# Kernel tuning notes

Hardware: AMD Instinct MI355X
Metric: run time of the kernel (lower is better)

## Reference

```python
import jax, jax.numpy as jnp
import numpy as np

# ---------------- Chu-Liu-Edmonds MST decode (faithful numpy port) ----------------

def _find_cycle(parents, length, current_nodes):
    added = [False] * length
    added[0] = True
    cycle = set()
    has_cycle = False
    for i in range(1, length):
        if has_cycle:
            break
        if added[i] or not current_nodes[i]:
            continue
        this_cycle = {i}
        added[i] = True
        has_cycle = True
        next_node = i
        while parents[next_node] not in this_cycle:
            next_node = parents[next_node]
            if added[next_node]:
                has_cycle = False
                break
            added[next_node] = True
            this_cycle.add(next_node)
        if has_cycle:
            original = next_node
            cycle.add(original)
            next_node = parents[original]
            while next_node != original:
                cycle.add(next_node)
                next_node = parents[next_node]
            break
    return has_cycle, list(cycle)


def chu_liu_edmonds(length, score_matrix, current_nodes, final_edges, old_input, old_output, representatives):
    parents = [-1]
    for node1 in range(1, length):
        parents.append(0)
        if current_nodes[node1]:
            max_score = score_matrix[0, node1]
            for node2 in range(1, length):
                if node2 == node1 or not current_nodes[node2]:
                    continue
                new_score = score_matrix[node2, node1]
                if new_score > max_score:
                    max_score = new_score
                    parents[node1] = node2
    has_cycle, cycle = _find_cycle(parents, length, current_nodes)
    if not has_cycle:
        final_edges[0] = -1
        for node in range(1, length):
            if not current_nodes[node]:
                continue
            parent = old_input[parents[node], node]
            child = old_output[parents[node], node]
            final_edges[child] = parent
        return
    cycle_weight = 0.0
    for node in cycle:
        cycle_weight += score_matrix[parents[node], node]
    cycle_representative = cycle[0]
    for node in range(length):
        if not current_nodes[node] or node in cycle:
            continue
        in_edge_weight = float('-inf')
        in_edge = -1
        out_edge_weight = float('-inf')
        out_edge = -1
        for node_in_cycle in cycle:
            if score_matrix[node_in_cycle, node] > in_edge_weight:
                in_edge_weight = score_matrix[node_in_cycle, node]
                in_edge = node_in_cycle
            score = cycle_weight + score_matrix[node, node_in_cycle] - score_matrix[parents[node_in_cycle], node_in_cycle]
            if score > out_edge_weight:
                out_edge_weight = score
                out_edge = node_in_cycle
        score_matrix[cycle_representative, node] = in_edge_weight
        old_input[cycle_representative, node] = old_input[in_edge, node]
        old_output[cycle_representative, node] = old_output[in_edge, node]
        score_matrix[node, cycle_representative] = out_edge_weight
        old_output[node, cycle_representative] = old_output[node, out_edge]
        old_input[node, cycle_representative] = old_input[node, out_edge]
    considered = []
    for i, node_in_cycle in enumerate(cycle):
        considered.append(set())
        if i > 0:
            current_nodes[node_in_cycle] = False
        for node in representatives[node_in_cycle]:
            considered[i].add(node)
            if i > 0:
                representatives[cycle_representative].add(node)
    chu_liu_edmonds(length, score_matrix, current_nodes, final_edges, old_input, old_output, representatives)
    found = False
    key_node = -1
    for i, node in enumerate(cycle):
        for cycle_rep in considered[i]:
            if cycle_rep in final_edges:
                key_node = node
                found = True
                break
        if found:
            break
    previous = parents[key_node]
    while previous != key_node:
        child = old_output[parents[previous], previous]
        parent = old_input[parents[previous], previous]
        final_edges[child] = parent
        previous = parents[previous]


def decode_mst(energy, length):
    # energy: numpy [num_labels, T, T]
    max_length = energy.shape[-1]
    energy = energy[:, :length, :length]
    label_id_matrix = energy.argmax(axis=0)
    score_matrix = np.array(energy.max(axis=0), copy=True)
    old_input = np.zeros([length, length], dtype=np.int32)
    old_output = np.zeros([length, length], dtype=np.int32)
    current_nodes = [True] * length
    representatives = []
    for node1 in range(length):
        score_matrix[node1, node1] = 0.0
        representatives.append({node1})
        for node2 in range(node1 + 1, length):
            old_input[node1, node2] = node1
            old_output[node1, node2] = node2
            old_input[node2, node1] = node2
            old_output[node2, node1] = node1
    final_edges = {}
    chu_liu_edmonds(length, score_matrix, current_nodes, final_edges, old_input, old_output, representatives)
    heads = np.zeros([max_length], np.int32)
    head_type = np.ones([max_length], np.int32)
    for child, parent in final_edges.items():
        heads[child] = parent
        head_type[child] = label_id_matrix[parent, child]
    return heads, head_type


# ---------------- biaffine scoring (jax) ----------------

@jax.jit
def _energy(encoded_text, W_head_arc, b_head_arc, W_dep_arc, b_dep_arc, U_arc,
            W_head_lab, b_head_lab, W_dep_lab, b_dep_lab, U_lab):
    h_arc = jax.nn.elu(encoded_text @ W_head_arc + b_head_arc)   # [B,T,A]
    d_arc = jax.nn.elu(encoded_text @ W_dep_arc + b_dep_arc)     # [B,T,A]
    arc_scores = jnp.einsum('bia,ac,bjc->bij', h_arc, U_arc, d_arc)  # head i -> dep j
    h_lab = jax.nn.elu(encoded_text @ W_head_lab + b_head_lab)   # [B,T,R]
    d_lab = jax.nn.elu(encoded_text @ W_dep_lab + b_dep_lab)     # [B,T,R]
    lab_scores = jnp.einsum('bir,lrs,bjs->blij', h_lab, U_lab, d_lab)  # [B,L,T,T]
    norm_arc = jax.nn.log_softmax(arc_scores, axis=1)   # normalize over heads
    norm_lab = jax.nn.log_softmax(lab_scores, axis=1)   # normalize over labels
    return jnp.exp(norm_arc[:, None, :, :] + norm_lab)  # [B,L,T,T] edge energies


def setup_inputs() -> dict:
    key = jax.random.key(0)
    ks = jax.random.split(key, 8)
    B, T, D, A, R, L = 32, 128, 768, 512, 128, 50
    s = 0.02
    return {
        'encoded_text': jax.random.normal(ks[0], (B, T, D), jnp.float32),
        'W_head_arc': jax.random.normal(ks[1], (D, A), jnp.float32) * s,
        'b_head_arc': jnp.zeros((A,), jnp.float32),
        'W_dep_arc': jax.random.normal(ks[2], (D, A), jnp.float32) * s,
        'b_dep_arc': jnp.zeros((A,), jnp.float32),
        'U_arc': jax.random.normal(ks[3], (A, A), jnp.float32) * s,
        'W_head_lab': jax.random.normal(ks[4], (D, R), jnp.float32) * s,
        'b_head_lab': jnp.zeros((R,), jnp.float32),
        'W_dep_lab': jax.random.normal(ks[5], (D, R), jnp.float32) * s,
        'b_dep_lab': jnp.zeros((R,), jnp.float32),
        'U_lab': jax.random.normal(ks[6], (L, R, R), jnp.float32) * s,
        'mask': jnp.ones((B, T), jnp.bool_),
    }


def reference(encoded_text, W_head_arc, b_head_arc, W_dep_arc, b_dep_arc, U_arc,
              W_head_lab, b_head_lab, W_dep_lab, b_dep_lab, U_lab, mask):
    energy = _energy(encoded_text, W_head_arc, b_head_arc, W_dep_arc, b_dep_arc, U_arc,
                     W_head_lab, b_head_lab, W_dep_lab, b_dep_lab, U_lab)
    lengths = np.asarray(mask.sum(-1))
    energy_np = np.asarray(energy)
    heads, tags = [], []
    # per-example Chu-Liu-Edmonds decode (inherently sequential, as in the original)
    for i in range(energy_np.shape[0]):
        h, t = decode_mst(energy_np[i], int(lengths[i]))
        heads.append(h)
        tags.append(t)
    return energy, jnp.asarray(np.stack(heads)), jnp.asarray(np.stack(tags))
```

## Files before the change

### kernel.cpp

```cpp
#include <hip/hip_runtime.h>
#include <math.h>

#define B_ 32
#define T_ 128
#define D_ 768
#define A_ 512
#define R_ 128
#define L_ 50

__global__ __launch_bounds__(256)
void proj_gemm_k(const float* __restrict__ X,
                 const float* __restrict__ Wha, const float* __restrict__ bha,
                 const float* __restrict__ Wda, const float* __restrict__ bda,
                 const float* __restrict__ Whl, const float* __restrict__ bhl,
                 const float* __restrict__ Wdl, const float* __restrict__ bdl,
                 float* __restrict__ HA, float* __restrict__ DA,
                 float* __restrict__ HL, float* __restrict__ DL)
{
    __shared__ float As[16][68];
    __shared__ float Bs[16][132];
    const int bx = blockIdx.x;
    const float *W, *bias; float* C; int ld, ncol;
    if (bx < 4)      { W = Wha; bias = bha; C = HA; ld = 512; ncol = bx * 128; }
    else if (bx < 8) { W = Wda; bias = bda; C = DA; ld = 512; ncol = (bx - 4) * 128; }
// ... 165 lines not shown
    for (int i = 0; i < T_; ++i) base[(size_t)i * T_] -= ls;
}

__global__ __launch_bounds__(256)
void lab_inplace_k(float* __restrict__ E, const float* __restrict__ dlt)
{
    __shared__ __align__(16) float As[T_ * R_];
    int l = blockIdx.x, b = blockIdx.y;
    float* base = E + ((size_t)b * L_ + l) * T_ * T_;
    int tid = threadIdx.x;
#pragma unroll
    for (int it = 0; it < 16; ++it) {
        int idx = (it * 256 + tid) * 4;
        *(float4*)&As[idx] = *(const float4*)&base[idx];
    }
    __syncthreads();
    int tx = tid & 15, ty = tid >> 4;
    int j0 = tx * 8, i0 = ty * 8;
    const float* dl = dlt + (size_t)b * T_ * R_;
    float acc[8][8] = {};
    for (int s0 = 0; s0 < R_; s0 += 4) {
        float a[8][4], bb[4][8];
#pragma unroll
        for (int ii = 0; ii < 8; ++ii) {
            float4 v = *(const float4*)&As[(i0 + ii) * R_ + s0];
            a[ii][0] = v.x; a[ii][1] = v.y; a[ii][2] = v.z; a[ii][3] = v.w;
        }
#pragma unroll
        for (int ss = 0; ss < 4; ++ss) {
            float4 x = *(const float4*)&dl[(size_t)(s0 + ss) * T_ + j0];
            float4 y = *(const float4*)&dl[(size_t)(s0 + ss) * T_ + j0 + 4];
            bb[ss][0] = x.x; bb[ss][1] = x.y; bb[ss][2] = x.z; bb[ss][3] = x.w;
            bb[ss][4] = y.x; bb[ss][5] = y.y; bb[ss][6] = y.z; bb[ss][7] = y.w;
        }
#pragma unroll
        for (int ii = 0; ii < 8; ++ii)
#pragma unroll
            for (int jj = 0; jj < 8; ++jj)
#pragma unroll
                for (int ss = 0; ss < 4; ++ss)
                    acc[ii][jj] += a[ii][ss] * bb[ss][jj];
    }
#pragma unroll
    for (int ii = 0; ii < 8; ++ii) {
        float4 o0 = { acc[ii][0], acc[ii][1], acc[ii][2], acc[ii][3] };
        float4 o1 = { acc[ii][4], acc[ii][5], acc[ii][6], acc[ii][7] };
        *(float4*)&base[(size_t)(i0 + ii) * T_ + j0] = o0;
        *(float4*)&base[(size_t)(i0 + ii) * T_ + j0 + 4] = o1;
    }
}

__global__ __launch_bounds__(256)
void energy_combine_k(float* __restrict__ E, const float* __restrict__ narc,
                      float* __restrict__ score_g, unsigned char* __restrict__ labmax_g)
{
    int g = blockIdx.x * 256 + threadIdx.x;
    int b = g >> 14;
    int ij = g & 16383;
    float* base = E + (size_t)b * L_ * T_ * T_ + ij;
    float v[L_];
    float m = -INFINITY;
    int am = 0;
#pragma unroll
    for (int l = 0; l < L_; ++l) {
        v[l] = base[(size_t)l * T_ * T_];
        if (v[l] > m) { m = v[l]; am = l; }
    }
    float s = 0.0f;
#pragma unroll
    for (int l = 0; l < L_; ++l) s += expf(v[l] - m);
    float ls = m + logf(s);
    float na = narc[(size_t)b * T_ * T_ + ij];
#pragma unroll
    for (int l = 0; l < L_; ++l) base[(size_t)l * T_ * T_] = expf(na + v[l] - ls);
    int i = ij >> 7, j = ij & 127;
    score_g[(size_t)b * 16384 + ij] = (i == j) ? 0.0f : expf(na + m - ls);
    labmax_g[(size_t)b * 16384 + ij] = (unsigned char)am;
}

__global__ __launch_bounds__(256)
void mst_k(const float* __restrict__ score_g, const unsigned char* __restrict__ labmax_g,
           float* __restrict__ heads, float* __restrict__ tags)
{
    int b = blockIdx.x, t = threadIdx.x;
    __shared__ float score[128 * 128];
    __shared__ unsigned char oin[128 * 128];
    __shared__ unsigned char oout[128 * 128];
    __shared__ unsigned char pstL[128 * 128];
    __shared__ unsigned char tstL[128 * 128];
    __shared__ unsigned char cstL[128 * 128];
    __shared__ int parents[128];
    __shared__ int fe[128];
    __shared__ float pmx[128];
    __shared__ int pp[128];
    __shared__ float sub[128];
    __shared__ unsigned char cyc[128], oncyc[128], pstrow[128];

    volatile float* vscore = score;
    volatile int* vpar = parents;
    volatile int* vfe = fe;
    volatile unsigned char* vcyc = cyc;
    volatile unsigned char* voncyc = oncyc;
    volatile unsigned char* voin = oin;
    volatile unsigned char* voout = oout;
    volatile unsigned char* vpstrow = pstrow;
    volatile float* vsub = sub;
    volatile unsigned char* vcst = cstL;
    volatile unsigned char* vpst = pstL;
    volatile unsigned char* vtst = tstL;

    {
        const float4* src = (const float4*)(score_g + (size_t)b * 16384);
#pragma unroll
        for (int r = 0; r < 16; ++r)
            ((float4*)score)[r * 256 + t] = src[r * 256 + t];
    }
    {
        int row = t >> 1, half = t & 1;
        unsigned int tv = (unsigned int)row * 0x01010101u;
        unsigned int* oinw = (unsigned int*)&oin[row * 128];
        unsigned int* ooutw = (unsigned int*)&oout[row * 128];
#pragma unroll
        for (int w = 0; w < 16; ++w) {
            int idx = half * 16 + w;
            oinw[idx] = tv;
            ooutw[idx] = 0x03020100u + 0x04040404u * (unsigned int)idx;
        }
    }
    if (t < 128) { fe[t] = -2; oncyc[t] = 0; }
    __syncthreads();
    if (t < 128) {
        score[t * 128 + t] = -INFINITY;
        oin[t * 129] = 0; oout[t * 129] = 0;
    }
    __syncthreads();
    float mxl = 0.0f; int pl = 0;
    if (t >= 128) {
        int col = t - 128;
        float mx = -INFINITY; int pu = 64;
        if (col != 0) {
            mx = score[64 * 128 + col];
#pragma unroll 16
            for (int n2 = 65; n2 < 128; ++n2) {
                float sc = score[n2 * 128 + col];
                if (sc > mx) { mx = sc; pu = n2; }
            }
        }
        pmx[col] = mx; pp[col] = pu;
    } else if (t != 0) {
        mxl = score[t]; pl = 0;
#pragma unroll 16
        for (int n2 = 1; n2 < 64; ++n2) {
            float sc = score[n2 * 128 + t];
            if (sc > mxl) { mxl = sc; pl = n2; }
        }
    }
    __syncthreads();
    if (t == 0) parents[0] = -1;
    else if (t < 128) parents[t] = (pmx[t] > mxl) ? pp[t] : pl;
    __syncthreads();

    if (t < 64) {
        const int n0 = t, n1 = t + 64;
        int p0 = vpar[n0], p1 = vpar[n1];
        int c0 = 1, c1 = 1;
        int r0 = n0, r1 = n1;
        int lev = 0;
        int nact = 128;
        for (;;) {
            int rounds = 32 - __clz(nact - 1);
            int a0 = (n0 == 0 || !c0) ? 0 : p0;
            int a1 = (!c1) ? 0 : p1;
            int m0 = n0, m1 = n1;
            for (int s = 0; s < rounds; ++s) {
                int pk0 = (a0 << 7) | m0;
                int pk1 = (a1 << 7) | m1;
                int s0l = a0 & 63, s1l = a1 & 63;
                int q00 = __shfl(pk0, s0l, 64);
                int q01 = __shfl(pk1, s0l, 64);
                int q10 = __shfl(pk0, s1l, 64);
                int q11 = __shfl(pk1, s1l, 64);
                int g0 = (a0 & 64) ? q01 : q00;
                int g1 = (a1 & 64) ? q11 : q10;
                a0 = g0 >> 7; int gm0 = g0 & 127; m0 = gm0 < m0 ? gm0 : m0;
                a1 = g1 >> 7; int gm1 = g1 & 127; m1 = gm1 < m1 ? gm1 : m1;
            }
            int pred0 = (n0 >= 1) && c0 && (a0 != 0);
            int pred1 = c1 && (a1 != 0);
            unsigned long long bal0 = __ballot(pred0);
            unsigned long long bal1 = __ballot(pred1);
            if (bal0 == 0ull && bal1 == 0ull) {
                if (n0 == 0) vfe[0] = -1;
                else if (c0) {
                    int pa = voin[p0 * 128 + n0];
                    int ch = voout[p0 * 128 + n0];
                    vfe[ch] = pa;
                }
                if (c1) {
                    int pa = voin[p1 * 128 + n1];
                    int ch = voout[p1 * 128 + n1];
                    vfe[ch] = pa;
                }
                __threadfence_block();
                break;
            }
            unsigned char ep = (unsigned char)(lev + 1);
            if (pred0) voncyc[a0] = ep;
            if (pred1) voncyc[a1] = ep;
            __threadfence_block();
            int onc0 = (voncyc[n0] == ep);
            int onc1 = (voncyc[n1] == ep);
            unsigned long long ob0 = __ballot(onc0);
            unsigned long long ob1 = __ballot(onc1);
            const int rep = ob0 ? ((int)__ffsll((long long)ob0) - 1)
                                : (64 + (int)__ffsll((long long)ob1) - 1);
            int member0 = onc0 && (m0 == rep);
            int member1 = onc1 && (m1 == rep);
            unsigned long long mb0 = __ballot(member0);
            unsigned long long mb1 = __ballot(member1);
            int clen = (int)__popcll(mb0) + (int)__popcll(mb1);
            int rank0 = (int)__popcll(mb0 & ((1ull << n0) - 1ull));
            int rank1 = (int)__popcll(mb0) + (int)__popcll(mb1 & ((1ull << n0) - 1ull));
            float s0m = member0 ? vscore[p0 * 128 + n0] : 0.0f;
            float s1m = member1 ? vscore[p1 * 128 + n1] : 0.0f;
            if (member0) { vcyc[rank0] = (unsigned char)n0; vsub[rank0] = s0m;
                           vcst[lev * 128 + rank0] = (unsigned char)n0; }
            if (member1) { vcyc[rank1] = (unsigned char)n1; vsub[rank1] = s1m;
                           vcst[lev * 128 + rank1] = (unsigned char)n1; }
            vpst[lev * 128 + n0] = (unsigned char)p0;
            vpst[lev * 128 + n1] = (unsigned char)p1;
            int mbit_r0 = (r0 < 64) ? (int)((mb0 >> r0) & 1ull) : (int)((mb1 >> (r0 - 64)) & 1ull);
            int mbit_r1 = (r1 < 64) ? (int)((mb0 >> r1) & 1ull) : (int)((mb1 >> (r1 - 64)) & 1ull);
            int tg0 = mbit_r0 ? ((r0 < 64) ? (int)__popcll(mb0 & ((1ull << r0) - 1ull))
                                           : (int)__popcll(mb0) + (int)__popcll(mb1 & ((1ull << (r0 - 64)) - 1ull)))
                              : 0xFF;
            int tg1 = mbit_r1 ? ((r1 < 64) ? (int)__popcll(mb0 & ((1ull << r1) - 1ull))
                                           : (int)__popcll(mb0) + (int)__popcll(mb1 & ((1ull << (r1 - 64)) - 1ull)))
                              : 0xFF;
            vtst[lev * 128 + n0] = (unsigned char)tg0;
            vtst[lev * 128 + n1] = (unsigned char)tg1;
            __threadfence_block();
            float cw = 0.0f;
            for (int i = 0; i < clen; ++i) cw += vsub[i];
#pragma unroll
            for (int half = 0; half < 2; ++half) {
                int n = half ? n1 : n0;
                int cc = half ? c1 : c0;
                int mem = half ? member1 : member0;
                if (cc && !mem) {
                    float inw = -INFINITY, outw = -INFINITY;
                    int ine = 0, oute = 0;
                    for (int i = 0; i < clen; ++i) {
                        int nic = (int)vcyc[i];
                        float sb = vsub[i];
                        float si = vscore[nic * 128 + n];
                        if (si > inw) { inw = si; ine = nic; }
                        float so = cw + vscore[n * 128 + nic] - sb;
                        if (so > outw) { outw = so; oute = nic; }
                    }
                    vscore[rep * 128 + n] = inw;
                    voin[rep * 128 + n] = voin[ine * 128 + n];
                    voout[rep * 128 + n] = voout[ine * 128 + n];
                    vscore[n * 128 + rep] = outw;
                    voout[n * 128 + rep] = voout[n * 128 + oute];
                    voin[n * 128 + rep] = voin[n * 128 + oute];
                }
            }
            __threadfence_block();
            if (member0 && n0 != rep) c0 = 0;
            if (member1 && n1 != rep) c1 = 0;
            if (tg0 != 0xFF) r0 = rep;
            if (tg1 != 0xFF) r1 = rep;
            int mbit_p0 = (p0 < 64) ? (int)((mb0 >> p0) & 1ull) : (int)((mb1 >> (p0 - 64)) & 1ull);
            int mbit_p1 = (p1 < 64) ? (int)((mb0 >> p1) & 1ull) : (int)((mb1 >> (p1 - 64)) & 1ull);
            if (c0 && n0 != 0 && n0 != rep && mbit_p0) p0 = rep;
            if (c1 && n1 != rep && mbit_p1) p1 = rep;
            {
                float cv0 = c0 ? vscore[n0 * 128 + rep] : -INFINITY;
                float cv1 = c1 ? vscore[n1 * 128 + rep] : -INFINITY;
                float bv; int bi;
                if (cv1 > cv0) { bv = cv1; bi = n1; } else { bv = cv0; bi = n0; }
#pragma unroll
                for (int off = 32; off >= 1; off >>= 1) {
                    float ov = __shfl_xor(bv, off, 64);
                    int oi = __shfl_xor(bi, off, 64);
                    if (ov > bv || (ov == bv && oi < bi)) { bv = ov; bi = oi; }
                }
                if (n0 == rep) p0 = bi;
                if (n1 == rep) p1 = bi;
            }
            nact -= (clen - 1);
            ++lev;
        }
        for (int l2 = lev - 1; l2 >= 0; --l2) {
            int q0 = vpst[l2 * 128 + n0], q1 = vpst[l2 * 128 + n1];
            vpstrow[n0] = (unsigned char)q0;
            vpstrow[n1] = (unsigned char)q1;
            int tg0 = vtst[l2 * 128 + n0], tg1 = vtst[l2 * 128 + n1];
            int kf0 = (tg0 != 0xFF) && (vfe[n0] != -2);
            int kf1 = (tg1 != 0xFF) && (vfe[n1] != -2);
            int kv0 = kf0 ? (int)vcst[l2 * 128 + tg0] : 0;
            int kv1 = kf1 ? (int)vcst[l2 * 128 + tg1] : 0;
            unsigned long long kb0 = __ballot(kf0);
            unsigned long long kb1 = __ballot(kf1);
            int key = -1;
            if (kb0)      key = __shfl(kv0, (int)__ffsll((long long)kb0) - 1, 64);
            else if (kb1) key = __shfl(kv1, (int)__ffsll((long long)kb1) - 1, 64);
            __threadfence_block();
            if (t == 0 && key >= 0) {
                int prev = (int)vpstrow[key];
                int guard = 0;
                while (prev != key && guard++ < 200) {
                    int pp2 = (int)vpstrow[prev];
                    int ch = (int)voout[pp2 * 128 + prev];
                    int pa = (int)voin[pp2 * 128 + prev];
                    vfe[ch] = pa;
                    prev = pp2;
                }
            }
            __threadfence_block();
        }
    }
    __syncthreads();

    if (t < 128) {
        int f = fe[t];
        float h, ht;
        if (f != -2) {
            h = (float)f;
            int prow = (f < 0) ? 127 : f;
            ht = (float)(int)labmax_g[(size_t)b * 16384 + prow * 128 + t];
        } else { h = 0.0f; ht = 1.0f; }
        heads[b * 128 + t] = h;
        tags[b * 128 + t] = ht;
    }
}

extern "C" void kernel_launch(void* const* d_in, const int* in_sizes, int n_in,
                              void* d_out, int out_size, void* d_ws, size_t ws_size,
                              hipStream_t stream)
{
    const float* X   = (const float*)d_in[0];
    const float* Wha = (const float*)d_in[1];
    const float* bha = (const float*)d_in[2];
    const float* Wda = (const float*)d_in[3];
    const float* bda = (const float*)d_in[4];
    const float* Ua  = (const float*)d_in[5];
    const float* Whl = (const float*)d_in[6];
    const float* bhl = (const float*)d_in[7];
    const float* Wdl = (const float*)d_in[8];
    const float* bdl = (const float*)d_in[9];
    const float* Ul  = (const float*)d_in[10];

    char* ws = (char*)d_ws;
    float* HA    = (float*)(ws + (size_t)0);
    float* DA    = (float*)(ws + ((size_t)8 << 20));
    float* TA    = (float*)(ws + ((size_t)16 << 20));
    float* HL    = (float*)(ws + ((size_t)24 << 20));
    float* DL    = (float*)(ws + ((size_t)26 << 20));
    float* DLt   = (float*)(ws + ((size_t)28 << 20));
    float* ARC   = (float*)(ws + ((size_t)30 << 20));
    float* SCORE = (float*)(ws + ((size_t)32 << 20));
    unsigned char* LABMAX = (unsigned char*)(ws + ((size_t)34 << 20));

    float* E     = (float*)d_out;
    float* heads = E + (size_t)B_ * L_ * T_ * T_;
    float* tags  = heads + (size_t)B_ * T_;

    dim3 thr(256);
    proj_gemm_k<<<dim3(10, 64), thr, 0, stream>>>(X, Wha, bha, Wda, bda, Whl, bhl, Wdl, bdl,
                                                  HA, DA, HL, DL);
    gemm_k<<<dim3(4, 64, 1), thr, 0, stream>>>(HA, Ua, nullptr, TA, 512, 512, 512, 512, 0, 0, 0, (long long)128 * 512, 0);
    transpose_k<<<dim3(4, 4, 32), dim3(32, 8), 0, stream>>>(DL, DLt);
    gemm_k<<<dim3(1, 2, 32), thr, 0, stream>>>(TA, DA, nullptr, ARC, 512, 512, 512, 128, 65536, 65536, 16384, 0, 4);
    arc_logsoftmax_k<<<32, 128, 0, stream>>>(ARC);
    gemm_k<<<dim3(1, 64, 50), thr, 0, stream>>>(HL, Ul, nullptr, E, 128, 128, 128, 128, 0, 16384, 16384, (long long)50 * 16384, 0);
    lab_inplace_k<<<dim3(50, 32), thr, 0, stream>>>(E, DLt);
    energy_combine_k<<<2048, 256, 0, stream>>>(E, ARC, SCORE, LABMAX);
    mst_k<<<32, 256, 0, stream>>>(SCORE, LABMAX, heads, tags);
}
```

Baseline: 942.5 us.

## Contract all cycles per MST round and pad shared score matrix rows

Reworks the Chu-Liu-Edmonds loop so each iteration contracts every detected cycle at once instead of only the first. Cycle members are grouped by cycle id using atomics and a wave prefix scan, and in/out edge weights are recomputed per segment. Parents are then re-selected for contracted nodes. Shared matrices are padded to a 129 stride to avoid LDS bank conflicts on column walks. The aim is fewer sequential contraction rounds, at the cost of more complex per-round work and atomics, plus a risk of diverging from the reference's tie-breaking or cycle-choice order.

```diff
diff --git a/kernel.cpp b/kernel.cpp
--- a/kernel.cpp
+++ b/kernel.cpp
@@ -271,67 +271,66 @@
 void mst_k(const float* __restrict__ score_g, const unsigned char* __restrict__ labmax_g,
            float* __restrict__ heads, float* __restrict__ tags)
 {
-    int b = blockIdx.x, t = threadIdx.x;
-    __shared__ float score[128 * 128];
-    __shared__ unsigned char oin[128 * 128];
-    __shared__ unsigned char oout[128 * 128];
+    const int b = blockIdx.x, t = threadIdx.x;
+    __shared__ float score[128 * 129];
+    __shared__ unsigned char oin[128 * 129];
+    __shared__ unsigned char oout[128 * 129];
     __shared__ unsigned char pstL[128 * 128];
-    __shared__ unsigned char tstL[128 * 128];
-    __shared__ unsigned char cstL[128 * 128];
+    __shared__ unsigned char kynL[128 * 128];
     __shared__ int parents[128];
     __shared__ int fe[128];
     __shared__ float pmx[128];
     __shared__ int pp[128];
-    __shared__ float sub[128];
-    __shared__ unsigned char cyc[128], oncyc[128], pstrow[128];
+    __shared__ float cwacc[128];
+    __shared__ int cnt[128];
+    __shared__ int offarr[128];
+    __shared__ float Lsub[128];
+    __shared__ unsigned char Lnode[128], Lcid[128];
+    __shared__ unsigned char cidarr[128], actarr[128], oncyc[128];
 
     volatile float* vscore = score;
-    volatile int* vpar = parents;
-    volatile int* vfe = fe;
-    volatile unsigned char* vcyc = cyc;
-    volatile unsigned char* voncyc = oncyc;
     volatile unsigned char* voin = oin;
     volatile unsigned char* voout = oout;
-    volatile unsigned char* vpstrow = pstrow;
-    volatile float* vsub = sub;
-    volatile unsigned char* vcst = cstL;
     volatile unsigned char* vpst = pstL;
-    volatile unsigned char* vtst = tstL;
+    volatile unsigned char* vkyn = kynL;
+    volatile int* vfe = fe;
+    volatile float* vcw = cwacc;
+    volatile int* vcnt = cnt;
+    volatile int* voff = offarr;
+    volatile float* vLs = Lsub;
+    volatile unsigned char* vLn = Lnode;
+    volatile unsigned char* vLc = Lcid;
+    volatile unsigned char* vcid = cidarr;
+    volatile unsigned char* vact = actarr;
+    volatile unsigned char* vonc = oncyc;
 
     {
         const float4* src = (const float4*)(score_g + (size_t)b * 16384);
-#pragma unroll
-        for (int r = 0; r < 16; ++r)
-            ((float4*)score)[r * 256 + t] = src[r * 256 + t];
-    }
-    {
-        int row = t >> 1, half = t & 1;
-        unsigned int tv = (unsigned int)row * 0x01010101u;
-        unsigned int* oinw = (unsigned int*)&oin[row * 128];
-        unsigned int* ooutw = (unsigned int*)&oout[row * 128];
-#pragma unroll
-        for (int w = 0; w < 16; ++w) {
-            int idx = half * 16 + w;
-            oinw[idx] = tv;
-            ooutw[idx] = 0x03020100u + 0x04040404u * (unsigned int)idx;
-        }
-    }
-    if (t < 128) { fe[t] = -2; oncyc[t] = 0; }
-    __syncthreads();
-    if (t < 128) {
-        score[t * 128 + t] = -INFINITY;
-        oin[t * 129] = 0; oout[t * 129] = 0;
-    }
+        for (int i = t; i < 4096; i += 256) {
+            float4 v = src[i];
+            int r = i >> 5, c = (i & 31) * 4;
+            float* d = &score[r * 129 + c];
+            d[0] = v.x; d[1] = v.y; d[2] = v.z; d[3] = v.w;
+        }
+    }
+    for (int i = t; i < 16384; i += 256) {
+        int r = i >> 7, c = i & 127;
+        oin[r * 129 + c] = (unsigned char)r;
+        oout[r * 129 + c] = (unsigned char)c;
+    }
+    if (t < 128) { fe[t] = -2; oncyc[t] = 0; actarr[t] = 1; }
+    __syncthreads();
+    if (t < 128) score[t * 129 + t] = -INFINITY;
     __syncthreads();
     float mxl = 0.0f; int pl = 0;
     if (t >= 128) {
         int col = t - 128;
         float mx = -INFINITY; int pu = 64;
         if (col != 0) {
-            mx = score[64 * 128 + col];
+            mx = score[64 * 129 + col];
 #pragma unroll 16
             for (int n2 = 65; n2 < 128; ++n2) {
-                float sc = score[n2 * 128 + col];
+                float sc = score[n2 * 129 + col];
                 if (sc > mx) { mx = sc; pu = n2; }
             }
         }
@@ -340,7 +339,7 @@
         mxl = score[t]; pl = 0;
 #pragma unroll 16
         for (int n2 = 1; n2 < 64; ++n2) {
-            float sc = score[n2 * 128 + t];
+            float sc = score[n2 * 129 + t];
             if (sc > mxl) { mxl = sc; pl = n2; }
         }
     }
@@ -351,11 +350,10 @@
 
     if (t < 64) {
         const int n0 = t, n1 = t + 64;
-        int p0 = vpar[n0], p1 = vpar[n1];
+        int p0 = parents[n0], p1 = parents[n1];
         int c0 = 1, c1 = 1;
         int r0 = n0, r1 = n1;
-        int lev = 0;
-        int nact = 128;
+        int lev = 0, nact = 128;
         for (;;) {
             int rounds = 32 - __clz(nact - 1);
             int a0 = (n0 == 0 || !c0) ? 0 : p0;
@@ -380,130 +378,161 @@
             unsigned long long bal1 = __ballot(pred1);
             if (bal0 == 0ull && bal1 == 0ull) {
                 if (n0 == 0) vfe[0] = -1;
-                else if (c0) {
-                    int pa = voin[p0 * 128 + n0];
-                    int ch = voout[p0 * 128 + n0];
-                    vfe[ch] = pa;
-                }
-                if (c1) {
-                    int pa = voin[p1 * 128 + n1];
-                    int ch = voout[p1 * 128 + n1];
-                    vfe[ch] = pa;
-                }
+                else if (c0) vfe[voout[p0 * 129 + n0]] = voin[p0 * 129 + n0];
+                if (c1) vfe[voout[p1 * 129 + n1]] = voin[p1 * 129 + n1];
                 __threadfence_block();
                 break;
             }
             unsigned char ep = (unsigned char)(lev + 1);
-            if (pred0) voncyc[a0] = ep;
-            if (pred1) voncyc[a1] = ep;
-            __threadfence_block();
-            int onc0 = (voncyc[n0] == ep);
-            int onc1 = (voncyc[n1] == ep);
-            unsigned long long ob0 = __ballot(onc0);
-            unsigned long long ob1 = __ballot(onc1);
-            const int rep = ob0 ? ((int)__ffsll((long long)ob0) - 1)
-                                : (64 + (int)__ffsll((long long)ob1) - 1);
-            int member0 = onc0 && (m0 == rep);
-            int member1 = onc1 && (m1 == rep);
-            unsigned long long mb0 = __ballot(member0);
-            unsigned long long mb1 = __ballot(member1);
-            int clen = (int)__popcll(mb0) + (int)__popcll(mb1);
-            int rank0 = (int)__popcll(mb0 & ((1ull << n0) - 1ull));
-            int rank1 = (int)__popcll(mb0) + (int)__popcll(mb1 & ((1ull << n0) - 1ull));
-            float s0m = member0 ? vscore[p0 * 128 + n0] : 0.0f;
-            float s1m = member1 ? vscore[p1 * 128 + n1] : 0.0f;
-            if (member0) { vcyc[rank0] = (unsigned char)n0; vsub[rank0] = s0m;
-                           vcst[lev * 128 + rank0] = (unsigned char)n0; }
-            if (member1) { vcyc[rank1] = (unsigned char)n1; vsub[rank1] = s1m;
-                           vcst[lev * 128 + rank1] = (unsigned char)n1; }
+            if (pred0) vonc[a0] = ep;
+            if (pred1) vonc[a1] = ep;
+            vcnt[n0] = 0; vcnt[n1] = 0;
+            vcw[n0] = 0.0f; vcw[n1] = 0.0f;
+            __threadfence_block();
+            int onc0 = c0 && (vonc[n0] == ep);
+            int onc1 = c1 && (vonc[n1] == ep);
+            int cid0 = m0, cid1 = m1;
+            vcid[n0] = onc0 ? (unsigned char)cid0 : 0xFF;
+            vcid[n1] = onc1 ? (unsigned char)cid1 : 0xFF;
+            float sub0 = 0.0f, sub1 = 0.0f;
+            int rk0 = 0, rk1 = 0;
+            if (onc0) { sub0 = vscore[p0 * 129 + n0]; rk0 = atomicAdd(&cnt[cid0], 1); atomicAdd(&cwacc[cid0], sub0); }
+            if (onc1) { sub1 = vscore[p1 * 129 + n1]; rk1 = atomicAdd(&cnt[cid1], 1); atomicAdd(&cwacc[cid1], sub1); }
+            __threadfence_block();
+            int x0 = vcnt[n0], x1 = vcnt[n1];
+            int v = (x0 & 0xFFFF) | (x1 << 16);
+            for (int off = 1; off < 64; off <<= 1) {
+                int srcl = t >= off ? t - off : 0;
+                int u = __shfl(v, srcl, 64);
+                v += (t >= off) ? u : 0;
+            }
+            int tot = __shfl(v, 63, 64);
+            int Mtot = (tot & 0xFFFF) + (tot >> 16);
+            voff[n0] = (v & 0xFFFF) - x0;
+            voff[n1] = (tot & 0xFFFF) + ((v >> 16) & 0xFFFF) - x1;
+            __threadfence_block();
+            if (onc0) { int sl = voff[cid0] + rk0; vLn[sl] = (unsigned char)n0; vLc[sl] = (unsigned char)cid0; vLs[sl] = sub0; }
+            if (onc1) { int sl = voff[cid1] + rk1; vLn[sl] = (unsigned char)n1; vLc[sl] = (unsigned char)cid1; vLs[sl] = sub1; }
             vpst[lev * 128 + n0] = (unsigned char)p0;
             vpst[lev * 128 + n1] = (unsigned char)p1;
-            int mbit_r0 = (r0 < 64) ? (int)((mb0 >> r0) & 1ull) : (int)((mb1 >> (r0 - 64)) & 1ull);
-            int mbit_r1 = (r1 < 64) ? (int)((mb0 >> r1) & 1ull) : (int)((mb1 >> (r1 - 64)) & 1ull);
-            int tg0 = mbit_r0 ? ((r0 < 64) ? (int)__popcll(mb0 & ((1ull << r0) - 1ull))
-                                           : (int)__popcll(mb0) + (int)__popcll(mb1 & ((1ull << (r0 - 64)) - 1ull)))
-                              : 0xFF;
-            int tg1 = mbit_r1 ? ((r1 < 64) ? (int)__popcll(mb0 & ((1ull << r1) - 1ull))
-                                           : (int)__popcll(mb0) + (int)__popcll(mb1 & ((1ull << (r1 - 64)) - 1ull)))
-                              : 0xFF;
-            vtst[lev * 128 + n0] = (unsigned char)tg0;
-            vtst[lev * 128 + n1] = (unsigned char)tg1;
-            __threadfence_block();
-            float cw = 0.0f;
-            for (int i = 0; i < clen; ++i) cw += vsub[i];
-#pragma unroll
-            for (int half = 0; half < 2; ++half) {
-                int n = half ? n1 : n0;
-                int cc = half ? c1 : c0;
-                int mem = half ? member1 : member0;
-                if (cc && !mem) {
-                    float inw = -INFINITY, outw = -INFINITY;
-                    int ine = 0, oute = 0;
-                    for (int i = 0; i < clen; ++i) {
-                        int nic = (int)vcyc[i];
-                        float sb = vsub[i];
-                        float si = vscore[nic * 128 + n];
-                        if (si > inw) { inw = si; ine = nic; }
-                        float so = cw + vscore[n * 128 + nic] - sb;
-                        if (so > outw) { outw = so; oute = nic; }
+            int rc0 = vcid[r0], rc1 = vcid[r1];
+            vkyn[lev * 128 + n0] = (rc0 != 0xFF) ? (unsigned char)r0 : 0xFF;
+            vkyn[lev * 128 + n1] = (rc1 != 0xFF) ? (unsigned char)r1 : 0xFF;
+            if (rc0 != 0xFF) r0 = rc0;
+            if (rc1 != 0xFF) r1 = rc1;
+            __threadfence_block();
+            int cidn0 = onc0 ? cid0 : 0xFF;
+            int cidn1 = onc1 ? cid1 : 0xFF;
+            {
+                float ow0 = -INFINITY, ow1 = -INFINITY;
+                int oe0 = 0, oe1 = 0;
+                for (int i = 0; i < Mtot; ++i) {
+                    int cidI = vLc[i];
+                    int x = vLn[i];
+                    float sb = vLs[i];
+                    float so0 = vscore[n0 * 129 + x] - sb;
+                    float so1 = vscore[n1 * 129 + x] - sb;
+                    if (c0 && cidI != cidn0 && so0 > ow0) { ow0 = so0; oe0 = x; }
+                    if (c1 && cidI != cidn1 && so1 > ow1) { ow1 = so1; oe1 = x; }
+                    int segend = (i + 1 == Mtot) || ((int)vLc[i + 1] != cidI);
+                    if (segend) {
+                        float cwc = vcw[cidI];
+                        if (c0 && cidI != cidn0) {
+                            unsigned char too = voout[n0 * 129 + oe0], toi = voin[n0 * 129 + oe0];
+                            vscore[n0 * 129 + cidI] = cwc + ow0;
+                            voout[n0 * 129 + cidI] = too; voin[n0 * 129 + cidI] = toi;
+                        }
+                        if (c1 && cidI != cidn1) {
+                            unsigned char too = voout[n1 * 129 + oe1], toi = voin[n1 * 129 + oe1];
+                            vscore[n1 * 129 + cidI] = cwc + ow1;
+                            voout[n1 * 129 + cidI] = too; voin[n1 * 129 + cidI] = toi;
+                        }
+                        ow0 = -INFINITY; ow1 = -INFINITY; oe0 = 0; oe1 = 0;
                     }
-                    vscore[rep * 128 + n] = inw;
-                    voin[rep * 128 + n] = voin[ine * 128 + n];
-                    voout[rep * 128 + n] = voout[ine * 128 + n];
-                    vscore[n * 128 + rep] = outw;
-                    voout[n * 128 + rep] = voout[n * 128 + oute];
-                    voin[n * 128 + rep] = voin[n * 128 + oute];
                 }
             }
             __threadfence_block();
-            if (member0 && n0 != rep) c0 = 0;
-            if (member1 && n1 != rep) c1 = 0;
-            if (tg0 != 0xFF) r0 = rep;
-            if (tg1 != 0xFF) r1 = rep;
-            int mbit_p0 = (p0 < 64) ? (int)((mb0 >> p0) & 1ull) : (int)((mb1 >> (p0 - 64)) & 1ull);
-            int mbit_p1 = (p1 < 64) ? (int)((mb0 >> p1) & 1ull) : (int)((mb1 >> (p1 - 64)) & 1ull);
-            if (c0 && n0 != 0 && n0 != rep && mbit_p0) p0 = rep;
-            if (c1 && n1 != rep && mbit_p1) p1 = rep;
             {
-                float cv0 = c0 ? vscore[n0 * 128 + rep] : -INFINITY;
-                float cv1 = c1 ? vscore[n1 * 128 + rep] : -INFINITY;
-                float bv; int bi;
-                if (cv1 > cv0) { bv = cv1; bi = n1; } else { bv = cv0; bi = n0; }
-#pragma unroll
-                for (int off = 32; off >= 1; off >>= 1) {
-                    float ov = __shfl_xor(bv, off, 64);
-                    int oi = __shfl_xor(bi, off, 64);
-                    if (ov > bv || (ov == bv && oi < bi)) { bv = ov; bi = oi; }
+                float iw0 = -INFINITY, iw1 = -INFINITY;
+                int ie0 = 0, ie1 = 0;
+                for (int i = 0; i < Mtot; ++i) {
+                    int cidI = vLc[i];
+                    int x = vLn[i];
+                    float si0 = vscore[x * 129 + n0];
+                    float si1 = vscore[x * 129 + n1];
+                    if (c0 && cidI != cidn0 && si0 > iw0) { iw0 = si0; ie0 = x; }
+                    if (c1 && cidI != cidn1 && si1 > iw1) { iw1 = si1; ie1 = x; }
+                    int segend = (i + 1 == Mtot) || ((int)vLc[i + 1] != cidI);
+                    if (segend) {
+                        if (c0 && cidI != cidn0) {
+                            unsigned char too = voout[ie0 * 129 + n0], toi = voin[ie0 * 129 + n0];
+                            vscore[cidI * 129 + n0] = iw0;
+                            voout[cidI * 129 + n0] = too; voin[cidI * 129 + n0] = toi;
+                        }
+                        if (c1 && cidI != cidn1) {
+                            unsigned char too = voout[ie1 * 129 + n1], toi = voin[ie1 * 129 + n1];
+                            vscore[cidI * 129 + n1] = iw1;
+                            voout[cidI * 129 + n1] = too; voin[cidI * 129 + n1] = toi;
+                        }
+                        iw0 = -INFINITY; iw1 = -INFINITY; ie0 = 0; ie1 = 0;
+                    }
                 }
-                if (n0 == rep) p0 = bi;
-                if (n1 == rep) p1 = bi;
-            }
-            nact -= (clen - 1);
+            }
+            __threadfence_block();
+            if (onc0 && n0 != cid0) c0 = 0;
+            if (onc1 && n1 != cid1) c1 = 0;
+            vact[n0] = (unsigned char)c0;
+            vact[n1] = (unsigned char)c1;
+            if (c0 && n0 != 0) { int cp = vcid[p0]; if (cp != 0xFF) p0 = cp; }
+            if (c1)            { int cp = vcid[p1]; if (cp != 0xFF) p1 = cp; }
+            __threadfence_block();
+            if (c0 && onc0) {
+                float mx = vscore[n0]; int par = 0;
+                for (int x2 = 1; x2 < 128; ++x2) {
+                    if (vact[x2] && x2 != n0) {
+                        float sc = vscore[x2 * 129 + n0];
+                        if (sc > mx) { mx = sc; par = x2; }
+                    }
+                }
+                p0 = par;
+            }
+            if (c1 && onc1) {
+                float mx = vscore[n1]; int par = 0;
+                for (int x2 = 1; x2 < 128; ++x2) {
+                    if (vact[x2] && x2 != n1) {
+                        float sc = vscore[x2 * 129 + n1];
+                        if (sc > mx) { mx = sc; par = x2; }
+                    }
+                }
+                p1 = par;
+            }
+            int ncyc = __popcll(__ballot(onc0 && n0 == cid0)) +
+                       __popcll(__ballot(onc1 && n1 == cid1));
+            nact -= (Mtot - ncyc);
             ++lev;
         }
         for (int l2 = lev - 1; l2 >= 0; --l2) {
-            int q0 = vpst[l2 * 128 + n0], q1 = vpst[l2 * 128 + n1];
-            vpstrow[n0] = (unsigned char)q0;
-            vpstrow[n1] = (unsigned char)q1;
-            int tg0 = vtst[l2 * 128 + n0], tg1 = vtst[l2 * 128 + n1];
-            int kf0 = (tg0 != 0xFF) && (vfe[n0] != -2);
-            int kf1 = (tg1 != 0xFF) && (vfe[n1] != -2);
-            int kv0 = kf0 ? (int)vcst[l2 * 128 + tg0] : 0;
-            int kv1 = kf1 ? (int)vcst[l2 * 128 + tg1] : 0;
-            unsigned long long kb0 = __ballot(kf0);
-            unsigned long long kb1 = __ballot(kf1);
-            int key = -1;
-            if (kb0)      key = __shfl(kv0, (int)__ffsll((long long)kb0) - 1, 64);
-            else if (kb1) key = __shfl(kv1, (int)__ffsll((long long)kb1) - 1, 64);
-            __threadfence_block();
-            if (t == 0 && key >= 0) {
-                int prev = (int)vpstrow[key];
+            int ky0 = vkyn[l2 * 128 + n0], ky1 = vkyn[l2 * 128 + n1];
+            int f0 = vfe[n0], f1 = vfe[n1];
+            int cand0 = (ky0 != 0xFF) && (f0 != -2);
+            int cand1 = (ky1 != 0xFF) && (f1 != -2);
+            if (cand0) {
+                int key = ky0;
+                int prev = vpst[l2 * 128 + key];
                 int guard = 0;
-                while (prev != key && guard++ < 200) {
-                    int pp2 = (int)vpstrow[prev];
-                    int ch = (int)voout[pp2 * 128 + prev];
-                    int pa = (int)voin[pp2 * 128 + prev];
-                    vfe[ch] = pa;
+                while (prev != key && guard++ < 130) {
+                    int pp2 = vpst[l2 * 128 + prev];
+                    vfe[voout[pp2 * 129 + prev]] = voin[pp2 * 129 + prev];
+                    prev = pp2;
+                }
+            }
+            if (cand1) {
+                int key = ky1;
+                int prev = vpst[l2 * 128 + key];
+                int guard = 0;
+                while (prev != key && guard++ < 130) {
+                    int pp2 = vpst[l2 * 128 + prev];
+                    vfe[voout[pp2 * 129 + prev]] = voin[pp2 * 129 + prev];
                     prev = pp2;
                 }
             }
```

Result: slower. 1.682 ms (+78.5%).

## Contract all cycles per pass, pack edge maps, pad score rows in MST

Applied to the files above, without the earlier changes.

Restructures the single-wavefront Chu-Liu-Edmonds decode. Each pass now contracts every cycle found rather than only the first, with a fast path for two-node cycles. The two byte edge-origin maps are packed into one 16-bit array, and the score and origin arrays get rows padded to 129 to avoid LDS bank conflicts on column reads. The cycle weight is now summed with a wave reduction, and unwinding runs per lane instead of through thread 0. This is meant to cut the number of serial contraction rounds and LDS traffic in a latency-bound kernel, at the cost of more complex bookkeeping and some risk of diverging from the reference tie-breaking.

```diff
diff --git a/kernel.cpp b/kernel.cpp
--- a/kernel.cpp
+++ b/kernel.cpp
@@ -271,67 +271,53 @@
 void mst_k(const float* __restrict__ score_g, const unsigned char* __restrict__ labmax_g,
            float* __restrict__ heads, float* __restrict__ tags)
 {
-    int b = blockIdx.x, t = threadIdx.x;
-    __shared__ float score[128 * 128];
-    __shared__ unsigned char oin[128 * 128];
-    __shared__ unsigned char oout[128 * 128];
+    const int b = blockIdx.x, t = threadIdx.x;
+    __shared__ float score[128 * 129];
+    __shared__ unsigned short oio[128 * 129];
     __shared__ unsigned char pstL[128 * 128];
-    __shared__ unsigned char tstL[128 * 128];
-    __shared__ unsigned char cstL[128 * 128];
+    __shared__ unsigned char kynL[128 * 128];
     __shared__ int parents[128];
     __shared__ int fe[128];
     __shared__ float pmx[128];
     __shared__ int pp[128];
     __shared__ float sub[128];
-    __shared__ unsigned char cyc[128], oncyc[128], pstrow[128];
+    __shared__ unsigned char cyc[128], oncyc[128];
 
     volatile float* vscore = score;
-    volatile int* vpar = parents;
+    volatile unsigned short* voio = oio;
+    volatile unsigned char* vpst = pstL;
+    volatile unsigned char* vkyn = kynL;
     volatile int* vfe = fe;
+    volatile float* vsub = sub;
     volatile unsigned char* vcyc = cyc;
-    volatile unsigned char* voncyc = oncyc;
-    volatile unsigned char* voin = oin;
-    volatile unsigned char* voout = oout;
-    volatile unsigned char* vpstrow = pstrow;
-    volatile float* vsub = sub;
-    volatile unsigned char* vcst = cstL;
-    volatile unsigned char* vpst = pstL;
-    volatile unsigned char* vtst = tstL;
+    volatile unsigned char* vonc = oncyc;
 
     {
         const float4* src = (const float4*)(score_g + (size_t)b * 16384);
-#pragma unroll
-        for (int r = 0; r < 16; ++r)
-            ((float4*)score)[r * 256 + t] = src[r * 256 + t];
-    }
-    {
-        int row = t >> 1, half = t & 1;
-        unsigned int tv = (unsigned int)row * 0x01010101u;
-        unsigned int* oinw = (unsigned int*)&oin[row * 128];
-        unsigned int* ooutw = (unsigned int*)&oout[row * 128];
-#pragma unroll
-        for (int w = 0; w < 16; ++w) {
-            int idx = half * 16 + w;
-            oinw[idx] = tv;
-            ooutw[idx] = 0x03020100u + 0x04040404u * (unsigned int)idx;
-        }
+        for (int i = t; i < 4096; i += 256) {
+            float4 v = src[i];
+            int r = i >> 5, c = (i & 31) * 4;
+            float* d = &score[r * 129 + c];
+            d[0] = v.x; d[1] = v.y; d[2] = v.z; d[3] = v.w;
+        }
+    }
+    for (int i = t; i < 16384; i += 256) {
+        int r = i >> 7, c = i & 127;
+        oio[r * 129 + c] = (unsigned short)(r | (c << 8));
     }
     if (t < 128) { fe[t] = -2; oncyc[t] = 0; }
     __syncthreads();
-    if (t < 128) {
-        score[t * 128 + t] = -INFINITY;
-        oin[t * 129] = 0; oout[t * 129] = 0;
-    }
+    if (t < 128) score[t * 129 + t] = -INFINITY;
     __syncthreads();
     float mxl = 0.0f; int pl = 0;
     if (t >= 128) {
         int col = t - 128;
         float mx = -INFINITY; int pu = 64;
         if (col != 0) {
-            mx = score[64 * 128 + col];
+            mx = score[64 * 129 + col];
 #pragma unroll 16
             for (int n2 = 65; n2 < 128; ++n2) {
-                float sc = score[n2 * 128 + col];
+                float sc = score[n2 * 129 + col];
                 if (sc > mx) { mx = sc; pu = n2; }
             }
         }
@@ -340,7 +326,7 @@
         mxl = score[t]; pl = 0;
 #pragma unroll 16
         for (int n2 = 1; n2 < 64; ++n2) {
-            float sc = score[n2 * 128 + t];
+            float sc = score[n2 * 129 + t];
             if (sc > mxl) { mxl = sc; pl = n2; }
         }
     }
@@ -351,11 +337,11 @@
 
     if (t < 64) {
         const int n0 = t, n1 = t + 64;
-        int p0 = vpar[n0], p1 = vpar[n1];
+        int p0 = parents[n0], p1 = parents[n1];
         int c0 = 1, c1 = 1;
         int r0 = n0, r1 = n1;
-        int lev = 0;
-        int nact = 128;
+        int lev = 0, nact = 128, pass = 0;
+        const unsigned long long lmask = (1ull << t) - 1ull;
         for (;;) {
             int rounds = 32 - __clz(nact - 1);
             int a0 = (n0 == 0 || !c0) ? 0 : p0;
@@ -364,11 +350,10 @@
             for (int s = 0; s < rounds; ++s) {
                 int pk0 = (a0 << 7) | m0;
                 int pk1 = (a1 << 7) | m1;
-                int s0l = a0 & 63, s1l = a1 & 63;
-                int q00 = __shfl(pk0, s0l, 64);
-                int q01 = __shfl(pk1, s0l, 64);
-                int q10 = __shfl(pk0, s1l, 64);
-                int q11 = __shfl(pk1, s1l, 64);
+                int q00 = __shfl(pk0, a0 & 63, 64);
+                int q01 = __shfl(pk1, a0 & 63, 64);
+                int q10 = __shfl(pk0, a1 & 63, 64);
+                int q11 = __shfl(pk1, a1 & 63, 64);
                 int g0 = (a0 & 64) ? q01 : q00;
                 int g1 = (a1 & 64) ? q11 : q10;
                 a0 = g0 >> 7; int gm0 = g0 & 127; m0 = gm0 < m0 ? gm0 : m0;
@@ -380,130 +365,164 @@
             unsigned long long bal1 = __ballot(pred1);
             if (bal0 == 0ull && bal1 == 0ull) {
                 if (n0 == 0) vfe[0] = -1;
-                else if (c0) {
-                    int pa = voin[p0 * 128 + n0];
-                    int ch = voout[p0 * 128 + n0];
-                    vfe[ch] = pa;
-                }
-                if (c1) {
-                    int pa = voin[p1 * 128 + n1];
-                    int ch = voout[p1 * 128 + n1];
-                    vfe[ch] = pa;
-                }
+                else if (c0) { int w = voio[p0 * 129 + n0]; vfe[w >> 8] = w & 255; }
+                if (c1) { int w = voio[p1 * 129 + n1]; vfe[w >> 8] = w & 255; }
                 __threadfence_block();
                 break;
             }
-            unsigned char ep = (unsigned char)(lev + 1);
-            if (pred0) voncyc[a0] = ep;
-            if (pred1) voncyc[a1] = ep;
+            unsigned char ep = (unsigned char)(++pass);
+            if (pred0) vonc[a0] = ep;
+            if (pred1) vonc[a1] = ep;
             __threadfence_block();
-            int onc0 = (voncyc[n0] == ep);
-            int onc1 = (voncyc[n1] == ep);
-            unsigned long long ob0 = __ballot(onc0);
-            unsigned long long ob1 = __ballot(onc1);
-            const int rep = ob0 ? ((int)__ffsll((long long)ob0) - 1)
-                                : (64 + (int)__ffsll((long long)ob1) - 1);
-            int member0 = onc0 && (m0 == rep);
-            int member1 = onc1 && (m1 == rep);
-            unsigned long long mb0 = __ballot(member0);
-            unsigned long long mb1 = __ballot(member1);
-            int clen = (int)__popcll(mb0) + (int)__popcll(mb1);
-            int rank0 = (int)__popcll(mb0 & ((1ull << n0) - 1ull));
-            int rank1 = (int)__popcll(mb0) + (int)__popcll(mb1 & ((1ull << n0) - 1ull));
-            float s0m = member0 ? vscore[p0 * 128 + n0] : 0.0f;
-            float s1m = member1 ? vscore[p1 * 128 + n1] : 0.0f;
-            if (member0) { vcyc[rank0] = (unsigned char)n0; vsub[rank0] = s0m;
-                           vcst[lev * 128 + rank0] = (unsigned char)n0; }
-            if (member1) { vcyc[rank1] = (unsigned char)n1; vsub[rank1] = s1m;
-                           vcst[lev * 128 + rank1] = (unsigned char)n1; }
-            vpst[lev * 128 + n0] = (unsigned char)p0;
-            vpst[lev * 128 + n1] = (unsigned char)p1;
-            int mbit_r0 = (r0 < 64) ? (int)((mb0 >> r0) & 1ull) : (int)((mb1 >> (r0 - 64)) & 1ull);
-            int mbit_r1 = (r1 < 64) ? (int)((mb0 >> r1) & 1ull) : (int)((mb1 >> (r1 - 64)) & 1ull);
-            int tg0 = mbit_r0 ? ((r0 < 64) ? (int)__popcll(mb0 & ((1ull << r0) - 1ull))
-                                           : (int)__popcll(mb0) + (int)__popcll(mb1 & ((1ull << (r0 - 64)) - 1ull)))
-                              : 0xFF;
-            int tg1 = mbit_r1 ? ((r1 < 64) ? (int)__popcll(mb0 & ((1ull << r1) - 1ull))
-                                           : (int)__popcll(mb0) + (int)__popcll(mb1 & ((1ull << (r1 - 64)) - 1ull)))
-                              : 0xFF;
-            vtst[lev * 128 + n0] = (unsigned char)tg0;
-            vtst[lev * 128 + n1] = (unsigned char)tg1;
-            __threadfence_block();
-            float cw = 0.0f;
-            for (int i = 0; i < clen; ++i) cw += vsub[i];
-#pragma unroll
-            for (int half = 0; half < 2; ++half) {
-                int n = half ? n1 : n0;
-                int cc = half ? c1 : c0;
-                int mem = half ? member1 : member0;
-                if (cc && !mem) {
-                    float inw = -INFINITY, outw = -INFINITY;
-                    int ine = 0, oute = 0;
-                    for (int i = 0; i < clen; ++i) {
-                        int nic = (int)vcyc[i];
-                        float sb = vsub[i];
-                        float si = vscore[nic * 128 + n];
-                        if (si > inw) { inw = si; ine = nic; }
-                        float so = cw + vscore[n * 128 + nic] - sb;
-                        if (so > outw) { outw = so; oute = nic; }
+            int onc0 = c0 && (vonc[n0] == ep);
+            int onc1 = c1 && (vonc[n1] == ep);
+            const int cid0 = m0, cid1 = m1;
+            unsigned long long rm0 = __ballot(onc0 && n0 == cid0);
+            unsigned long long rm1 = __ballot(onc1 && n1 == cid1);
+            while (rm0 | rm1) {
+                int rep;
+                if (rm0) { rep = (int)__ffsll((long long)rm0) - 1; rm0 &= rm0 - 1; }
+                else     { rep = 64 + (int)__ffsll((long long)rm1) - 1; rm1 &= rm1 - 1; }
+                int member0 = onc0 && (cid0 == rep);
+                int member1 = onc1 && (cid1 == rep);
+                unsigned long long mb0 = __ballot(member0);
+                unsigned long long mb1 = __ballot(member1);
+                int clen = (int)__popcll(mb0) + (int)__popcll(mb1);
+                vpst[lev * 128 + n0] = (unsigned char)p0;
+                vpst[lev * 128 + n1] = (unsigned char)p1;
+                int mbr0 = (r0 < 64) ? (int)((mb0 >> r0) & 1ull) : (int)((mb1 >> (r0 - 64)) & 1ull);
+                int mbr1 = (r1 < 64) ? (int)((mb0 >> r1) & 1ull) : (int)((mb1 >> (r1 - 64)) & 1ull);
+                vkyn[lev * 128 + n0] = mbr0 ? (unsigned char)r0 : 0xFF;
+                vkyn[lev * 128 + n1] = mbr1 ? (unsigned char)r1 : 0xFF;
+                if (mbr0) r0 = rep;
+                if (mbr1) r1 = rep;
+                if (clen == 2) {
+                    unsigned long long ob0 = mb0, ob1 = mb1;
+                    if (rep < 64) ob0 &= ~(1ull << rep); else ob1 &= ~(1ull << (rep - 64));
+                    int v = ob0 ? (int)__ffsll((long long)ob0) - 1
+                                : 64 + (int)__ffsll((long long)ob1) - 1;
+                    int u = rep;
+                    int act0 = c0 && !member0;
+                    int act1 = c1 && !member1;
+                    float subU = vscore[v * 129 + u];
+                    float subV = vscore[u * 129 + v];
+                    float siU0 = 0, siV0 = 0, soU0 = 0, soV0 = 0;
+                    int ioiU0 = 0, ioiV0 = 0, iooU0 = 0, iooV0 = 0;
+                    float siU1 = 0, siV1 = 0, soU1 = 0, soV1 = 0;
+                    int ioiU1 = 0, ioiV1 = 0, iooU1 = 0, iooV1 = 0;
+                    if (act0) {
+                        siU0 = vscore[u * 129 + n0]; siV0 = vscore[v * 129 + n0];
+                        soU0 = vscore[n0 * 129 + u]; soV0 = vscore[n0 * 129 + v];
+                        ioiU0 = voio[u * 129 + n0]; ioiV0 = voio[v * 129 + n0];
+                        iooU0 = voio[n0 * 129 + u]; iooV0 = voio[n0 * 129 + v];
                     }
-                    vscore[rep * 128 + n] = inw;
-                    voin[rep * 128 + n] = voin[ine * 128 + n];
-                    voout[rep * 128 + n] = voout[ine * 128 + n];
-                    vscore[n * 128 + rep] = outw;
-                    voout[n * 128 + rep] = voout[n * 128 + oute];
-                    voin[n * 128 + rep] = voin[n * 128 + oute];
+                    if (act1) {
+                        siU1 = vscore[u * 129 + n1]; siV1 = vscore[v * 129 + n1];
+                        soU1 = vscore[n1 * 129 + u]; soV1 = vscore[n1 * 129 + v];
+                        ioiU1 = voio[u * 129 + n1]; ioiV1 = voio[v * 129 + n1];
+                        iooU1 = voio[n1 * 129 + u]; iooV1 = voio[n1 * 129 + v];
+                    }
+                    float cw = subU + subV;
+                    if (act0) {
+                        float inw; int ioi;
+                        if (siV0 > siU0) { inw = siV0; ioi = ioiV0; } else { inw = siU0; ioi = ioiU0; }
+                        float oU = soU0 - subU, oV = soV0 - subV;
+                        float outw; int ioo;
+                        if (oV > oU) { outw = oV; ioo = iooV0; } else { outw = oU; ioo = iooU0; }
+                        vscore[u * 129 + n0] = inw;       voio[u * 129 + n0] = (unsigned short)ioi;
+                        vscore[n0 * 129 + u] = cw + outw; voio[n0 * 129 + u] = (unsigned short)ioo;
+                    }
+                    if (act1) {
+                        float inw; int ioi;
+                        if (siV1 > siU1) { inw = siV1; ioi = ioiV1; } else { inw = siU1; ioi = ioiU1; }
+                        float oU = soU1 - subU, oV = soV1 - subV;
+                        float outw; int ioo;
+                        if (oV > oU) { outw = oV; ioo = iooV1; } else { outw = oU; ioo = iooU1; }
+                        vscore[u * 129 + n1] = inw;       voio[u * 129 + n1] = (unsigned short)ioi;
+                        vscore[n1 * 129 + u] = cw + outw; voio[n1 * 129 + u] = (unsigned short)ioo;
+                    }
+                } else {
+                    int rank0 = (int)__popcll(mb0 & lmask);
+                    int rank1 = (int)__popcll(mb0) + (int)__popcll(mb1 & lmask);
+                    float s0m = member0 ? vscore[p0 * 129 + n0] : 0.0f;
+                    float s1m = member1 ? vscore[p1 * 129 + n1] : 0.0f;
+                    if (member0) { vcyc[rank0] = (unsigned char)n0; vsub[rank0] = s0m; }
+                    if (member1) { vcyc[rank1] = (unsigned char)n1; vsub[rank1] = s1m; }
+                    __threadfence_block();
+                    float cw = s0m + s1m;
+#pragma unroll
+                    for (int off = 32; off >= 1; off >>= 1) cw += __shfl_xor(cw, off, 64);
+#pragma unroll
+                    for (int half = 0; half < 2; ++half) {
+                        int n = half ? n1 : n0;
+                        int act = half ? (c1 && !member1) : (c0 && !member0);
+                        if (act) {
+                            float inw = -INFINITY, outw = -INFINITY;
+                            int ine = 0, oute = 0;
+                            for (int i = 0; i < clen; ++i) {
+                                int nic = (int)vcyc[i];
+                                float sb = vsub[i];
+                                float si = vscore[nic * 129 + n];
+                                if (si > inw) { inw = si; ine = nic; }
+                                float so = cw + vscore[n * 129 + nic] - sb;
+                                if (so > outw) { outw = so; oute = nic; }
+                            }
+                            vscore[rep * 129 + n] = inw;
+                            voio[rep * 129 + n] = voio[ine * 129 + n];
+                            vscore[n * 129 + rep] = outw;
+                            voio[n * 129 + rep] = voio[n * 129 + oute];
+                        }
+                    }
+                }
+                __threadfence_block();
+                if (member0 && n0 != rep) c0 = 0;
+                if (member1 && n1 != rep) c1 = 0;
+                int mbp0 = (p0 >= 0 && p0 < 64) ? (int)((mb0 >> p0) & 1ull)
+                                                : (p0 >= 64 ? (int)((mb1 >> (p0 - 64)) & 1ull) : 0);
+                int mbp1 = (p1 < 64) ? (int)((mb0 >> p1) & 1ull) : (int)((mb1 >> (p1 - 64)) & 1ull);
+                if (c0 && n0 != 0 && mbp0) p0 = rep;
+                if (c1 && mbp1) p1 = rep;
+                {
+                    float cv0 = c0 ? vscore[n0 * 129 + rep] : -INFINITY;
+                    float cv1 = c1 ? vscore[n1 * 129 + rep] : -INFINITY;
+                    float bv; int bi;
+                    if (cv1 > cv0) { bv = cv1; bi = n1; } else { bv = cv0; bi = n0; }
+#pragma unroll
+                    for (int off = 32; off >= 1; off >>= 1) {
+                        float ov = __shfl_xor(bv, off, 64);
+                        int oi = __shfl_xor(bi, off, 64);
+                        if (ov > bv || (ov == bv && oi < bi)) { bv = ov; bi = oi; }
+                    }
+                    if (n0 == rep) p0 = bi;
+                    if (n1 == rep) p1 = bi;
+                }
+                nact -= (clen - 1);
+                ++lev;
+            }
+        }
+        for (int l2 = lev - 1; l2 >= 0; --l2) {
+            int ky0 = vkyn[l2 * 128 + n0], ky1 = vkyn[l2 * 128 + n1];
+            int cand0 = (ky0 != 0xFF) && (vfe[n0] != -2);
+            int cand1 = (ky1 != 0xFF) && (vfe[n1] != -2);
+            if (cand0) {
+                int key = ky0;
+                int prev = vpst[l2 * 128 + key];
+                int guard = 0;
+                while (prev != key && guard++ < 130) {
+                    int pp2 = vpst[l2 * 128 + prev];
+                    int w = voio[pp2 * 129 + prev];
+                    vfe[w >> 8] = w & 255;
+                    prev = pp2;
                 }
             }
-            __threadfence_block();
-            if (member0 && n0 != rep) c0 = 0;
-            if (member1 && n1 != rep) c1 = 0;
-            if (tg0 != 0xFF) r0 = rep;
-            if (tg1 != 0xFF) r1 = rep;
-            int mbit_p0 = (p0 < 64) ? (int)((mb0 >> p0) & 1ull) : (int)((mb1 >> (p0 - 64)) & 1ull);
-            int mbit_p1 = (p1 < 64) ? (int)((mb0 >> p1) & 1ull) : (int)((mb1 >> (p1 - 64)) & 1ull);
-            if (c0 && n0 != 0 && n0 != rep && mbit_p0) p0 = rep;
-            if (c1 && n1 != rep && mbit_p1) p1 = rep;
-            {
-                float cv0 = c0 ? vscore[n0 * 128 + rep] : -INFINITY;
-                float cv1 = c1 ? vscore[n1 * 128 + rep] : -INFINITY;
-                float bv; int bi;
-                if (cv1 > cv0) { bv = cv1; bi = n1; } else { bv = cv0; bi = n0; }
-#pragma unroll
-                for (int off = 32; off >= 1; off >>= 1) {
-                    float ov = __shfl_xor(bv, off, 64);
-                    int oi = __shfl_xor(bi, off, 64);
-                    if (ov > bv || (ov == bv && oi < bi)) { bv = ov; bi = oi; }
-                }
-                if (n0 == rep) p0 = bi;
-                if (n1 == rep) p1 = bi;
-            }
-            nact -= (clen - 1);
-            ++lev;
-        }
-        for (int l2 = lev - 1; l2 >= 0; --l2) {
-            int q0 = vpst[l2 * 128 + n0], q1 = vpst[l2 * 128 + n1];
-            vpstrow[n0] = (unsigned char)q0;
-            vpstrow[n1] = (unsigned char)q1;
-            int tg0 = vtst[l2 * 128 + n0], tg1 = vtst[l2 * 128 + n1];
-            int kf0 = (tg0 != 0xFF) && (vfe[n0] != -2);
-            int kf1 = (tg1 != 0xFF) && (vfe[n1] != -2);
-            int kv0 = kf0 ? (int)vcst[l2 * 128 + tg0] : 0;
-            int kv1 = kf1 ? (int)vcst[l2 * 128 + tg1] : 0;
-            unsigned long long kb0 = __ballot(kf0);
-            unsigned long long kb1 = __ballot(kf1);
-            int key = -1;
-            if (kb0)      key = __shfl(kv0, (int)__ffsll((long long)kb0) - 1, 64);
-            else if (kb1) key = __shfl(kv1, (int)__ffsll((long long)kb1) - 1, 64);
-            __threadfence_block();
-            if (t == 0 && key >= 0) {
-                int prev = (int)vpstrow[key];
+            if (cand1) {
+                int key = ky1;
+                int prev = vpst[l2 * 128 + key];
                 int guard = 0;
-                while (prev != key && guard++ < 200) {
-                    int pp2 = (int)vpstrow[prev];
-                    int ch = (int)voout[pp2 * 128 + prev];
-                    int pa = (int)voin[pp2 * 128 + prev];
-                    vfe[ch] = pa;
+                while (prev != key && guard++ < 130) {
+                    int pp2 = vpst[l2 * 128 + prev];
+                    int w = voio[pp2 * 129 + prev];
+                    vfe[w >> 8] = w & 255;
                     prev = pp2;
                 }
             }
```

New measurement: 887.0 us. -5.9%, faster.
